# Optimization experiments

Hardware: AMD Instinct MI355X
Metric: run time of the kernel (lower is better)

Reference implementation:

```python
import jax, jax.numpy as jnp
import numpy as np

N = 100000
E = 600000
NODE_DIM = 128
EDGE_DIM = 32
HIDDEN = 128  # must equal NODE_DIM (index_add_ into zeros_like(node_features))


def _linear_params(key, fan_in, fan_out):
    kw, kb = jax.random.split(key)
    bound = 1.0 / np.sqrt(fan_in)
    W = jax.random.uniform(kw, (fan_in, fan_out), minval=-bound, maxval=bound, dtype=jnp.float32)
    b = jax.random.uniform(kb, (fan_out,), minval=-bound, maxval=bound, dtype=jnp.float32)
    return W, b


def setup_inputs() -> dict:
    key = jax.random.key(0)
    ks = jax.random.split(key, 8)
    node_features = jax.random.normal(ks[0], (N, NODE_DIM), dtype=jnp.float32)
    edge_index = jax.random.randint(ks[1], (2, E), 0, N, dtype=jnp.int32)
    edge_features = jax.random.normal(ks[2], (E, EDGE_DIM), dtype=jnp.float32)
    m_W1, m_b1 = _linear_params(ks[3], 2 * NODE_DIM + EDGE_DIM, HIDDEN)
    m_W2, m_b2 = _linear_params(ks[4], HIDDEN, HIDDEN)
    a_W, a_b = _linear_params(ks[5], HIDDEN, 1)
    u_W1, u_b1 = _linear_params(ks[6], NODE_DIM + HIDDEN, HIDDEN)
    u_W2, u_b2 = _linear_params(ks[7], HIDDEN, NODE_DIM)
    return {
        "node_features": node_features,
        "edge_features": edge_features,
        "m_W1": m_W1, "m_b1": m_b1, "m_W2": m_W2, "m_b2": m_b2,
        "a_W": a_W, "a_b": a_b,
        "u_W1": u_W1, "u_b1": u_b1, "u_W2": u_W2, "u_b2": u_b2,
        "edge_index": edge_index,
    }


def reference(node_features, edge_features, m_W1, m_b1, m_W2, m_b2,
              a_W, a_b, u_W1, u_b1, u_W2, u_b2, edge_index):
    row, col = edge_index[0], edge_index[1]
    # gather endpoints + edge feats -> [E, 2*node_dim + edge_dim]
    msg_in = jnp.concatenate([node_features[row], node_features[col], edge_features], axis=-1)
    # message MLP
    h = jax.nn.relu(msg_in @ m_W1 + m_b1)
    messages = h @ m_W2 + m_b2  # [E, hidden]
    # global softmax over all edges (dim=0), per attention column (width 1)
    attn = jax.nn.softmax(messages @ a_W + a_b, axis=0)  # [E, 1]
    messages = messages * attn
    # scatter-add into destination nodes
    aggregated = jax.ops.segment_sum(messages, col, num_segments=node_features.shape[0])
    # update MLP + residual
    upd_in = jnp.concatenate([node_features, aggregated], axis=-1)
    u = jax.nn.relu(upd_in @ u_W1 + u_b1)
    updated = u @ u_W2 + u_b2
    return updated + node_features
```

## Files before the change

kernel.cpp:

```cpp
#include <hip/hip_runtime.h>
#include <hip/hip_bf16.h>
#include <hip/hip_fp8.h>
#include <stdint.h>

#define NN 100000
#define NE 600000
#define ND 128
#define ED 32
#define HID 128
#define SCANB 391
#define NEB 4688

using short8 = __attribute__((ext_vector_type(8))) short;
using f32x4  = __attribute__((ext_vector_type(4))) float;
using f32x2  = __attribute__((ext_vector_type(2))) float;

__device__ __forceinline__ uint32_t f2bf(float f) {
  uint32_t u = __float_as_uint(f);
  return (u + 0x7FFFu + ((u >> 16) & 1u)) >> 16;
}
__device__ __forceinline__ float bf2f(uint32_t h) {
  return __uint_as_float(h << 16);
}
__device__ __forceinline__ short8 pack8(float4 a, float4 b) {
  short8 s;
  s[0] = (short)f2bf(a.x); s[1] = (short)f2bf(a.y);
  s[2] = (short)f2bf(a.z); s[3] = (short)f2bf(a.w);
  s[4] = (short)f2bf(b.x); s[5] = (short)f2bf(b.y);
  s[6] = (short)f2bf(b.z); s[7] = (short)f2bf(b.w);
  return s;
}

__device__ __forceinline__ uint8_t fp8_enc(float v) {
#if __has_builtin(__builtin_amdgcn_cvt_pk_fp8_f32)
  return (uint8_t)(__builtin_amdgcn_cvt_pk_fp8_f32(v, v, 0, false) & 0xFF);
#else
  __hip_fp8_e4m3 q(v);
  return q.__x;
#endif
}
__device__ __forceinline__ float2 fp8_dec2(uint32_t v) {
#if __has_builtin(__builtin_amdgcn_cvt_pk_f32_fp8)
  f32x2 r = __builtin_amdgcn_cvt_pk_f32_fp8((int)v, false);
  return make_float2(r[0], r[1]);
#else
  __hip_fp8_e4m3 qa, qb;
  qa.__x = (uint8_t)(v & 0xFF); qb.__x = (uint8_t)((v >> 8) & 0xFF);
  return make_float2((float)qa, (float)qb);
#endif
}
__device__ __forceinline__ long pack_fp8x8(float4 a, float4 b) {
  union { uint8_t u8[8]; long l; } u;
  u.u8[0] = fp8_enc(a.x); u.u8[1] = fp8_enc(a.y);
  u.u8[2] = fp8_enc(a.z); u.u8[3] = fp8_enc(a.w);
  u.u8[4] = fp8_enc(b.x); u.u8[5] = fp8_enc(b.y);
  u.u8[6] = fp8_enc(b.z); u.u8[7] = fp8_enc(b.w);
  return u.l;
}

__global__ __launch_bounds__(256) void k_prep_all(
    const float* __restrict__ uW1, const float* __restrict__ uW2,
    const float* __restrict__ W1, const float* __restrict__ W2,
    short* __restrict__ U1p, short* __restrict__ U2p,
    uint8_t* __restrict__ W1p8, uint8_t* __restrict__ W2p8) {
  int o = blockIdx.x * 256 + threadIdx.x;
  const float* src; int rel; int isFp8;
  short* dstS = nullptr; uint8_t* dst8 = nullptr;
  if (o < 32768)       { rel = o;         src = uW1; dstS = U1p;  isFp8 = 0; }
  else if (o < 49152)  { rel = o - 32768; src = uW2; dstS = U2p;  isFp8 = 0; }
  else if (o < 86016)  { rel = o - 49152; src = W1;  dst8 = W1p8; isFp8 = 1; }
  else if (o < 102400) { rel = o - 86016; src = W2;  dst8 = W2p8; isFp8 = 1; }
  else return;
  int j = rel & 7, c16 = (rel >> 3) & 15, g = (rel >> 7) & 3, nt = (rel >> 9) & 7, c = rel >> 12;
  int k = c * 32 + g * 8 + j, n = nt * 16 + c16;
  float v = src[k * 128 + n];
  if (isFp8) dst8[rel] = fp8_enc(v);
  else       dstS[rel] = (short)f2bf(v);
}

__global__ __launch_bounds__(256) void k_prep_nf(const float* __restrict__ nf,
                                                 short* __restrict__ nfb,
                                                 uint8_t* __restrict__ nfb8,
                                                 int* __restrict__ cnt) {
  const int total = NN * ND / 8;
  int gid = blockIdx.x * 256 + threadIdx.x;
  for (int i = gid; i < NN; i += gridDim.x * 256) cnt[i] = 0;
  for (int u = gid; u < total; u += gridDim.x * 256) {
    const float* s = nf + (size_t)u * 8;
    float4 v0 = *(const float4*)s, v1 = *(const float4*)(s + 4);
    *(short8*)(nfb + (size_t)u * 8) = pack8(v0, v1);
    uint8_t b[8];
    b[0] = fp8_enc(v0.x); b[1] = fp8_enc(v0.y); b[2] = fp8_enc(v0.z); b[3] = fp8_enc(v0.w);
    b[4] = fp8_enc(v1.x); b[5] = fp8_enc(v1.y); b[6] = fp8_enc(v1.z); b[7] = fp8_enc(v1.w);
    *(uint2*)(nfb8 + (size_t)u * 8) = *(const uint2*)b;
  }
}

__global__ __launch_bounds__(256, 4) void k_edge_mfma(
    const uint8_t* __restrict__ nfb8, const float* __restrict__ ef,
    const uint8_t* __restrict__ W1p8, const float* __restrict__ b1,
    const uint8_t* __restrict__ W2p8, const float* __restrict__ b2,
    const float* __restrict__ aW, const int* __restrict__ ei,
    const int* __restrict__ perm,
    uint8_t* __restrict__ msg8, float* __restrict__ logits) {
  __shared__ __align__(16) uint8_t sRow[128 * 136];
  __shared__ __align__(16) uint8_t sCol[128 * 136];
  __shared__ __align__(16) uint8_t sB8[4096];
  __shared__ int sIdx[256];
  __shared__ int sPerm[128];

  const int tid = threadIdx.x;
  const int wv = tid >> 6, ln = tid & 63, cr = ln & 15, gp = ln >> 4;
  const int e0 = blockIdx.x * 128;
  const int wrow = wv * 32;

  if (tid < 128) {
    int e = e0 + tid; if (e >= NE) e = NE - 1;
    sIdx[tid] = ei[e];
    sIdx[128 + tid] = ei[NE + e];
    sPerm[tid] = perm[e];
  }
  __syncthreads();

#pragma unroll
  for (int it = 0; it < 16; ++it) {
    int t = it * 256 + tid;
    int side = t >> 11;
    int r = (t & 2047) >> 4;
    int o = (t & 15) * 8;
    const uint8_t* src = nfb8 + (size_t)sIdx[side * 128 + r] * ND + o;
    uint8_t* dst = (side ? sCol : sRow) + r * 136 + o;
    *(uint2*)dst = *(const uint2*)src;
  }

  long efA0, efA1;
  {
    int ea = e0 + wrow + cr;      if (ea >= NE) ea = NE - 1;
    int eb = e0 + wrow + 16 + cr; if (eb >= NE) eb = NE - 1;
    const float* f0 = ef + (size_t)ea * ED + gp * 8;
    const float* f1 = ef + (size_t)eb * ED + gp * 8;
    efA0 = pack_fp8x8(*(const float4*)f0, *(const float4*)(f0 + 4));
    efA1 = pack_fp8x8(*(const float4*)f1, *(const float4*)(f1 + 4));
  }

  float bia[8], aWr[8], bia2[8];
#pragma unroll
  for (int nt = 0; nt < 8; ++nt) {
    bia[nt] = b1[nt * 16 + cr];
    bia2[nt] = b2[nt * 16 + cr];
    aWr[nt] = aW[nt * 16 + cr];
  }
  f32x4 acc[2][8];
#pragma unroll
  for (int mt = 0; mt < 2; ++mt)
#pragma unroll
    for (int nt = 0; nt < 8; ++nt)
      acc[mt][nt] = (f32x4){bia[nt], bia[nt], bia[nt], bia[nt]};

  for (int c = 0; c < 9; ++c) {
    __syncthreads();
    *(uint4*)&sB8[tid * 16] = *(const uint4*)(W1p8 + c * 4096 + tid * 16);
    __syncthreads();
    long af0, af1;
    if (c < 8) {
      const uint8_t* aSrc = (c < 4) ? (sRow + c * 32) : (sCol + (c - 4) * 32);
      af0 = *(const long*)(aSrc + (wrow + cr) * 136 + gp * 8);
      af1 = *(const long*)(aSrc + (wrow + 16 + cr) * 136 + gp * 8);
    } else {
      af0 = efA0; af1 = efA1;
    }
#pragma unroll
    for (int nt = 0; nt < 8; ++nt) {
      long bfr = *(const long*)&sB8[(nt * 4 + gp) * 128 + cr * 8];
      acc[0][nt] = __builtin_amdgcn_mfma_f32_16x16x32_fp8_fp8(af0, bfr, acc[0][nt], 0, 0, 0);
      acc[1][nt] = __builtin_amdgcn_mfma_f32_16x16x32_fp8_fp8(af1, bfr, acc[1][nt], 0, 0, 0);
    }
  }

#pragma unroll
  for (int mt = 0; mt < 2; ++mt)
#pragma unroll
    for (int nt = 0; nt < 8; ++nt)
#pragma unroll
      for (int rr = 0; rr < 4; ++rr)
        sRow[(wrow + mt * 16 + gp * 4 + rr) * 136 + nt * 16 + cr] =
            fp8_enc(fmaxf(acc[mt][nt][rr], 0.f));

  f32x4 acc2[2][8];
#pragma unroll
  for (int mt = 0; mt < 2; ++mt)
#pragma unroll
    for (int nt = 0; nt < 8; ++nt)
      acc2[mt][nt] = (f32x4){bia2[nt], bia2[nt], bia2[nt], bia2[nt]};
  for (int c2 = 0; c2 < 4; ++c2) {
    __syncthreads();
    *(uint4*)&sB8[tid * 16] = *(const uint4*)(W2p8 + c2 * 4096 + tid * 16);
    __syncthreads();
    long af0 = *(const long*)&sRow[(wrow + cr) * 136 + c2 * 32 + gp * 8];
    long af1 = *(const long*)&sRow[(wrow + 16 + cr) * 136 + c2 * 32 + gp * 8];
#pragma unroll
    for (int nt = 0; nt < 8; ++nt) {
      long bfr = *(const long*)&sB8[(nt * 4 + gp) * 128 + cr * 8];
      acc2[0][nt] = __builtin_amdgcn_mfma_f32_16x16x32_fp8_fp8(af0, bfr, acc2[0][nt], 0, 0, 0);
      acc2[1][nt] = __builtin_amdgcn_mfma_f32_16x16x32_fp8_fp8(af1, bfr, acc2[1][nt], 0, 0, 0);
    }
  }

#pragma unroll
  for (int mt = 0; mt < 2; ++mt)
#pragma unroll
    for (int rr = 0; rr < 4; ++rr) {
      float p = 0.f;
#pragma unroll
      for (int nt = 0; nt < 8; ++nt) p += acc2[mt][nt][rr] * aWr[nt];
      p += __shfl_xor(p, 1, 64);
      p += __shfl_xor(p, 2, 64);
      p += __shfl_xor(p, 4, 64);
      p += __shfl_xor(p, 8, 64);
      int row = wrow + mt * 16 + gp * 4 + rr;
      if (cr == 0 && e0 + row < NE) logits[sPerm[row]] = p;
    }

#pragma unroll
  for (int mt = 0; mt < 2; ++mt)
#pragma unroll
    for (int nt = 0; nt < 8; ++nt)
#pragma unroll
      for (int rr = 0; rr < 4; ++rr)
        sCol[(wrow + mt * 16 + gp * 4 + rr) * 136 + nt * 16 + cr] =
            fp8_enc(acc2[mt][nt][rr]);
  __syncthreads();
#pragma unroll
  for (int it = 0; it < 8; ++it) {
    int row = it * 16 + (tid >> 4), o8 = (tid & 15) * 8;
    if (e0 + row < NE)
      *(uint2*)(msg8 + (size_t)sPerm[row] * HID + o8) = *(const uint2*)&sCol[row * 136 + o8];
  }
}

__global__ __launch_bounds__(256, 4) void k_node_mfma(
    const short* __restrict__ nfb, const short* __restrict__ aggb,
    const short* __restrict__ U1p, const float* __restrict__ b1,
    const short* __restrict__ U2p, const float* __restrict__ b2,
    float* __restrict__ out) {
  __shared__ __align__(16) short sH[128 * 136];

  const int tid = threadIdx.x;
  const int wv = tid >> 6, ln = tid & 63, cr = ln & 15, gp = ln >> 4;
  const int n0 = blockIdx.x * 128;
  const int wrow = wv * 32;

  int na0 = n0 + wrow + cr;      if (na0 >= NN) na0 = NN - 1;
  int na1 = n0 + wrow + 16 + cr; if (na1 >= NN) na1 = NN - 1;

  float bia[8], bia2[8];
#pragma unroll
  for (int nt = 0; nt < 8; ++nt) {
    bia[nt] = b1[nt * 16 + cr];
    bia2[nt] = b2[nt * 16 + cr];
  }
  f32x4 acc[2][8];
#pragma unroll
  for (int mt = 0; mt < 2; ++mt)
#pragma unroll
    for (int nt = 0; nt < 8; ++nt)
      acc[mt][nt] = (f32x4){bia[nt], bia[nt], bia[nt], bia[nt]};

#pragma unroll
  for (int c = 0; c < 8; ++c) {
    const short* base = (c < 4) ? nfb : aggb;
    const int ko = (c & 3) * 32 + gp * 8;
    short8 af0 = *(const short8*)(base + (size_t)na0 * ND + ko);
    short8 af1 = *(const short8*)(base + (size_t)na1 * ND + ko);
    const short* Wc = U1p + c * 4096;
#pragma unroll
    for (int nt = 0; nt < 8; ++nt) {
      short8 bfr = *(const short8*)(Wc + (nt * 4 + gp) * 128 + cr * 8);
      acc[0][nt] = __builtin_amdgcn_mfma_f32_16x16x32_bf16(af0, bfr, acc[0][nt], 0, 0, 0);
      acc[1][nt] = __builtin_amdgcn_mfma_f32_16x16x32_bf16(af1, bfr, acc[1][nt], 0, 0, 0);
    }
  }

#pragma unroll
  for (int mt = 0; mt < 2; ++mt)
#pragma unroll
    for (int nt = 0; nt < 8; ++nt)
#pragma unroll
      for (int rr = 0; rr < 4; ++rr)
        sH[(wrow + mt * 16 + gp * 4 + rr) * 136 + nt * 16 + cr] =
            (short)f2bf(fmaxf(acc[mt][nt][rr], 0.f));

  f32x4 acc2[2][8];
#pragma unroll
  for (int mt = 0; mt < 2; ++mt)
#pragma unroll
    for (int nt = 0; nt < 8; ++nt)
      acc2[mt][nt] = (f32x4){bia2[nt], bia2[nt], bia2[nt], bia2[nt]};
#pragma unroll
  for (int c2 = 0; c2 < 4; ++c2) {
    short8 af0 = *(const short8*)&sH[(wrow + cr) * 136 + c2 * 32 + gp * 8];
    short8 af1 = *(const short8*)&sH[(wrow + 16 + cr) * 136 + c2 * 32 + gp * 8];
    const short* Wc = U2p + c2 * 4096;
#pragma unroll
    for (int nt = 0; nt < 8; ++nt) {
      short8 bfr = *(const short8*)(Wc + (nt * 4 + gp) * 128 + cr * 8);
      acc2[0][nt] = __builtin_amdgcn_mfma_f32_16x16x32_bf16(af0, bfr, acc2[0][nt], 0, 0, 0);
      acc2[1][nt] = __builtin_amdgcn_mfma_f32_16x16x32_bf16(af1, bfr, acc2[1][nt], 0, 0, 0);
    }
  }

#pragma unroll
  for (int mt = 0; mt < 2; ++mt)
#pragma unroll
    for (int rr = 0; rr < 4; ++rr) {
      int n = n0 + wrow + mt * 16 + gp * 4 + rr;
      if (n < NN) {
#pragma unroll
        for (int nt = 0; nt < 8; ++nt) {
          int col = nt * 16 + cr;
          float r = bf2f((uint16_t)nfb[(size_t)n * ND + col]);
          out[(size_t)n * ND + col] = acc2[mt][nt][rr] + r;
        }
      }
    }
}

__device__ __forceinline__ void ms_combine(float& m, float& s, float m2, float s2) {
  float M = fmaxf(m, m2);
  s = s * expf(m - M) + s2 * expf(m2 - M);
  m = M;
}
__device__ __forceinline__ void ms_block_reduce(float& m, float& s) {
#pragma unroll
  for (int o = 1; o < 64; o <<= 1) {
    float m2 = __shfl_xor(m, o, 64), s2 = __shfl_xor(s, o, 64);
    ms_combine(m, s, m2, s2);
  }
  __shared__ float sm[4], ss[4];
  if ((threadIdx.x & 63) == 0) { sm[threadIdx.x >> 6] = m; ss[threadIdx.x >> 6] = s; }
  __syncthreads();
  m = sm[0]; s = ss[0];
  ms_combine(m, s, sm[1], ss[1]);
  ms_combine(m, s, sm[2], ss[2]);
  ms_combine(m, s, sm[3], ss[3]);
}
__global__ __launch_bounds__(256) void k_red_p(const float* __restrict__ logits,
                                               float* __restrict__ pmax,
                                               float* __restrict__ psum) {
  float m = -3.402823466e38f, s = 0.f;
  for (int i = blockIdx.x * 256 + threadIdx.x; i < NE; i += 1024 * 256) {
    float l = logits[i];
    if (l <= m) s += expf(l - m);
    else { s = s * expf(m - l) + 1.f; m = l; }
  }
  ms_block_reduce(m, s);
  if (threadIdx.x == 0) { pmax[blockIdx.x] = m; psum[blockIdx.x] = s; }
}
__global__ __launch_bounds__(256) void k_red_f(const float* __restrict__ pmax,
                                               const float* __restrict__ psum,
                                               float* __restrict__ red) {
  float m = pmax[threadIdx.x], s = psum[threadIdx.x];
  ms_combine(m, s, pmax[threadIdx.x + 256], psum[threadIdx.x + 256]);
  ms_combine(m, s, pmax[threadIdx.x + 512], psum[threadIdx.x + 512]);
  ms_combine(m, s, pmax[threadIdx.x + 768], psum[threadIdx.x + 768]);
  ms_block_reduce(m, s);
  if (threadIdx.x == 0) { red[0] = m; red[1] = 1.0f / s; }
}

__global__ __launch_bounds__(256) void k_hist(const int* __restrict__ ei,
                                              int* __restrict__ cnt) {
  int e = blockIdx.x * 256 + threadIdx.x;
  if (e < NE) atomicAdd(&cnt[ei[NE + e]], 1);
}
__global__ __launch_bounds__(256) void k_scan_bsum(const int* __restrict__ cnt,
                                                   int* __restrict__ bsum) {
  int i = blockIdx.x * 256 + threadIdx.x;
  int v = (i < NN) ? cnt[i] : 0;
#pragma unroll
  for (int s = 1; s < 64; s <<= 1) v += __shfl_xor(v, s, 64);
  __shared__ int sv[4];
  if ((threadIdx.x & 63) == 0) sv[threadIdx.x >> 6] = v;
  __syncthreads();
  if (threadIdx.x == 0) bsum[blockIdx.x] = sv[0] + sv[1] + sv[2] + sv[3];
}
__global__ __launch_bounds__(512) void k_scan_boff(const int* __restrict__ bsum,
                                                   int* __restrict__ boff,
                                                   int* __restrict__ rowptr) {
  __shared__ int s[512];
  int t = threadIdx.x;
  int v = (t < SCANB) ? bsum[t] : 0;
  s[t] = v;
  __syncthreads();
  for (int off = 1; off < 512; off <<= 1) {
    int u = (t >= off) ? s[t - off] : 0;
    __syncthreads();
    s[t] += u;
    __syncthreads();
  }
  if (t < SCANB) boff[t] = s[t] - v;
  if (t == 0) rowptr[NN] = NE;
}
__global__ __launch_bounds__(256) void k_scan_final(int* __restrict__ cnt,
                                                    const int* __restrict__ boff,
                                                    int* __restrict__ rowptr) {
  __shared__ int s[256];
  int b = blockIdx.x, t = threadIdx.x, i = b * 256 + t;
  int v = (i < NN) ? cnt[i] : 0;
  s[t] = v;
  __syncthreads();
  for (int off = 1; off < 256; off <<= 1) {
    int u = (t >= off) ? s[t - off] : 0;
    __syncthreads();
    s[t] += u;
    __syncthreads();
  }
  int excl = s[t] - v + boff[b];
  if (i < NN) { rowptr[i] = excl; cnt[i] = excl; }
}
__global__ __launch_bounds__(256) void k_fill(const int* __restrict__ ei,
                                              int* __restrict__ cursor,
                                              int* __restrict__ perm) {
  int e = blockIdx.x * 256 + threadIdx.x;
  if (e >= NE) return;
  int c = ei[NE + e];
  int pos = atomicAdd(&cursor[c], 1);
  perm[e] = pos;
}

__global__ __launch_bounds__(256) void k_agg(
    const uint8_t* __restrict__ msg8, const float* __restrict__ logits,
    const int* __restrict__ rowptr, const float* __restrict__ red,
    short* __restrict__ aggb) {
  int n = blockIdx.x * 4 + (threadIdx.x >> 6);
  int lane = threadIdx.x & 63;
  if (n >= NN) return;
  float gm = red[0], inv = red[1];
  int i0 = rowptr[n], i1 = rowptr[n + 1];
  float a0 = 0.f, a1 = 0.f;
  for (int i = i0; i < i1; ++i) {
    float wt = expf(logits[i] - gm) * inv;
    uint32_t pk = *(const uint16_t*)(msg8 + (size_t)i * HID + lane * 2);
    float2 d = fp8_dec2(pk);
    a0 += wt * d.x;
    a1 += wt * d.y;
  }
  uint32_t packed = f2bf(a0) | (f2bf(a1) << 16);
  *(uint32_t*)(aggb + (size_t)n * ND + lane * 2) = packed;
}

extern "C" void kernel_launch(void* const* d_in, const int* in_sizes, int n_in,
                              void* d_out, int out_size, void* d_ws, size_t ws_size,
                              hipStream_t stream) {
  const float* nf  = (const float*)d_in[0];
  const float* ef  = (const float*)d_in[1];
  const float* mW1 = (const float*)d_in[2];
  const float* mb1 = (const float*)d_in[3];
  const float* mW2 = (const float*)d_in[4];
  const float* mb2 = (const float*)d_in[5];
  const float* aW  = (const float*)d_in[6];
  const float* uW1 = (const float*)d_in[8];
  const float* ub1 = (const float*)d_in[9];
  const float* uW2 = (const float*)d_in[10];
  const float* ub2 = (const float*)d_in[11];
  const int*   ei  = (const int*)d_in[12];
  float* out = (float*)d_out;

  char* ws = (char*)d_ws;
  uint8_t* msg8 = (uint8_t*)ws;
  float* logits = (float*)(ws + 76800000);
  float* pmax = (float*)(ws + 79200000);
  float* psum = pmax + 1024;
  float* red  = psum + 1024;
  uint8_t* W1p8 = (uint8_t*)(ws + 79208256);
  uint8_t* W2p8 = W1p8 + 36864;
  short* U1p = (short*)(W2p8 + 16384);
  short* U2p = U1p + 32768;
  int* rowptr = (int*)(ws + 79413056);
  int* cnt    = rowptr + (NN + 1);
  int* perm   = cnt + NN;
  int* bsum   = perm + NE;
  int* boff   = bsum + 512;
  short* nfb  = (short*)(ws + 82620000);
  uint8_t* nfb8 = (uint8_t*)(ws + 108220000);
  short* aggb = (short*)(ws + 121020000);

  k_prep_all<<<400, 256, 0, stream>>>(uW1, uW2, mW1, mW2, U1p, U2p, W1p8, W2p8);
  k_prep_nf<<<2048, 256, 0, stream>>>(nf, nfb, nfb8, cnt);
  k_hist<<<(NE + 255) / 256, 256, 0, stream>>>(ei, cnt);
  k_scan_bsum<<<SCANB, 256, 0, stream>>>(cnt, bsum);
  k_scan_boff<<<1, 512, 0, stream>>>(bsum, boff, rowptr);
  k_scan_final<<<SCANB, 256, 0, stream>>>(cnt, boff, rowptr);
  k_fill<<<(NE + 255) / 256, 256, 0, stream>>>(ei, cnt, perm);
  k_edge_mfma<<<NEB, 256, 0, stream>>>(nfb8, ef, W1p8, mb1, W2p8, mb2, aW, ei, perm,
                                       msg8, logits);
  k_red_p<<<1024, 256, 0, stream>>>(logits, pmax, psum);
  k_red_f<<<1, 256, 0, stream>>>(pmax, psum, red);
  k_agg<<<(NN + 3) / 4, 256, 0, stream>>>(msg8, logits, rowptr, red, aggb);
  k_node_mfma<<<(NN + 127) / 128, 256, 0, stream>>>(nfb, aggb, U1p, ub1, U2p, ub2, out);
}
```

Before: 294.8 us.

## Fuse aggregation into node MLP kernel and merge launch-heavy prep/reduce kernels

The CSR gather-aggregation now runs inside the node MLP kernel and writes bf16 aggregates to shared memory, so the aggb round-trip through global memory and the k_agg launch are gone. The histogram moves into k_prep_nf, and count zeroing moves into k_prep_all. The two-stage softmax reduction becomes one kernel in which the last block, found with an atomic counter, does the final combine. Together this removes several launches. The risk is lower parallelism in the aggregation: each wave now handles 32 nodes one after another, with only 782 blocks, instead of one node per wave across 25k blocks.

```diff
diff --git a/kernel.cpp b/kernel.cpp
--- a/kernel.cpp
+++ b/kernel.cpp
@@ -62,8 +62,11 @@
     const float* __restrict__ uW1, const float* __restrict__ uW2,
     const float* __restrict__ W1, const float* __restrict__ W2,
     short* __restrict__ U1p, short* __restrict__ U2p,
-    uint8_t* __restrict__ W1p8, uint8_t* __restrict__ W2p8) {
+    uint8_t* __restrict__ W1p8, uint8_t* __restrict__ W2p8,
+    int* __restrict__ cnt, int* __restrict__ counter) {
   int o = blockIdx.x * 256 + threadIdx.x;
+  if (o < NN) cnt[o] = 0;
+  if (o == 0) *counter = 0;
   const float* src; int rel; int isFp8;
   short* dstS = nullptr; uint8_t* dst8 = nullptr;
   if (o < 32768)       { rel = o;         src = uW1; dstS = U1p;  isFp8 = 0; }
@@ -81,10 +84,12 @@
 __global__ __launch_bounds__(256) void k_prep_nf(const float* __restrict__ nf,
                                                  short* __restrict__ nfb,
                                                  uint8_t* __restrict__ nfb8,
+                                                 const int* __restrict__ ei,
                                                  int* __restrict__ cnt) {
   const int total = NN * ND / 8;
   int gid = blockIdx.x * 256 + threadIdx.x;
-  for (int i = gid; i < NN; i += gridDim.x * 256) cnt[i] = 0;
+  for (int e = gid; e < NE; e += gridDim.x * 256)
+    atomicAdd(&cnt[ei[NE + e]], 1);
   for (int u = gid; u < total; u += gridDim.x * 256) {
     const float* s = nf + (size_t)u * 8;
     float4 v0 = *(const float4*)s, v1 = *(const float4*)(s + 4);
@@ -238,17 +243,36 @@
   }
 }
 
-__global__ __launch_bounds__(256, 4) void k_node_mfma(
-    const short* __restrict__ nfb, const short* __restrict__ aggb,
+__global__ __launch_bounds__(256, 4) void k_node_fused(
+    const short* __restrict__ nfb, const uint8_t* __restrict__ msg8,
+    const float* __restrict__ logits, const int* __restrict__ rowptr,
+    const float* __restrict__ red,
     const short* __restrict__ U1p, const float* __restrict__ b1,
     const short* __restrict__ U2p, const float* __restrict__ b2,
     float* __restrict__ out) {
-  __shared__ __align__(16) short sH[128 * 136];
+  __shared__ __align__(16) short sBuf[128 * 136];
 
   const int tid = threadIdx.x;
   const int wv = tid >> 6, ln = tid & 63, cr = ln & 15, gp = ln >> 4;
   const int n0 = blockIdx.x * 128;
   const int wrow = wv * 32;
+  const float gm = red[0], inv = red[1];
+
+  for (int j = 0; j < 32; ++j) {
+    int n = n0 + wrow + j;
+    if (n >= NN) break;
+    int i0 = rowptr[n], i1 = rowptr[n + 1];
+    float a0 = 0.f, a1 = 0.f;
+    for (int i = i0; i < i1; ++i) {
+      float wt = expf(logits[i] - gm) * inv;
+      uint32_t pk = *(const uint16_t*)(msg8 + (size_t)i * HID + ln * 2);
+      float2 d = fp8_dec2(pk);
+      a0 += wt * d.x;
+      a1 += wt * d.y;
+    }
+    uint32_t packed = f2bf(a0) | (f2bf(a1) << 16);
+    *(uint32_t*)&sBuf[(wrow + j) * 136 + ln * 2] = packed;
+  }
 
   int na0 = n0 + wrow + cr;      if (na0 >= NN) na0 = NN - 1;
   int na1 = n0 + wrow + 16 + cr; if (na1 >= NN) na1 = NN - 1;
@@ -268,10 +292,16 @@
 
 #pragma unroll
   for (int c = 0; c < 8; ++c) {
-    const short* base = (c < 4) ? nfb : aggb;
-    const int ko = (c & 3) * 32 + gp * 8;
-    short8 af0 = *(const short8*)(base + (size_t)na0 * ND + ko);
-    short8 af1 = *(const short8*)(base + (size_t)na1 * ND + ko);
+    short8 af0, af1;
+    if (c < 4) {
+      const int ko = c * 32 + gp * 8;
+      af0 = *(const short8*)(nfb + (size_t)na0 * ND + ko);
+      af1 = *(const short8*)(nfb + (size_t)na1 * ND + ko);
+    } else {
+      const int ko = (c - 4) * 32 + gp * 8;
+      af0 = *(const short8*)&sBuf[(wrow + cr) * 136 + ko];
+      af1 = *(const short8*)&sBuf[(wrow + 16 + cr) * 136 + ko];
+    }
     const short* Wc = U1p + c * 4096;
 #pragma unroll
     for (int nt = 0; nt < 8; ++nt) {
@@ -287,7 +317,7 @@
     for (int nt = 0; nt < 8; ++nt)
 #pragma unroll
       for (int rr = 0; rr < 4; ++rr)
-        sH[(wrow + mt * 16 + gp * 4 + rr) * 136 + nt * 16 + cr] =
+        sBuf[(wrow + mt * 16 + gp * 4 + rr) * 136 + nt * 16 + cr] =
             (short)f2bf(fmaxf(acc[mt][nt][rr], 0.f));
 
   f32x4 acc2[2][8];
@@ -298,8 +328,8 @@
       acc2[mt][nt] = (f32x4){bia2[nt], bia2[nt], bia2[nt], bia2[nt]};
 #pragma unroll
   for (int c2 = 0; c2 < 4; ++c2) {
-    short8 af0 = *(const short8*)&sH[(wrow + cr) * 136 + c2 * 32 + gp * 8];
-    short8 af1 = *(const short8*)&sH[(wrow + 16 + cr) * 136 + c2 * 32 + gp * 8];
+    short8 af0 = *(const short8*)&sBuf[(wrow + cr) * 136 + c2 * 32 + gp * 8];
+    short8 af1 = *(const short8*)&sBuf[(wrow + 16 + cr) * 136 + c2 * 32 + gp * 8];
     const short* Wc = U2p + c2 * 4096;
 #pragma unroll
     for (int nt = 0; nt < 8; ++nt) {
@@ -344,9 +374,11 @@
   ms_combine(m, s, sm[2], ss[2]);
   ms_combine(m, s, sm[3], ss[3]);
 }
-__global__ __launch_bounds__(256) void k_red_p(const float* __restrict__ logits,
-                                               float* __restrict__ pmax,
-                                               float* __restrict__ psum) {
+__global__ __launch_bounds__(256) void k_red(const float* __restrict__ logits,
+                                             float* __restrict__ pmax,
+                                             float* __restrict__ psum,
+                                             float* __restrict__ red,
+                                             int* __restrict__ counter) {
   float m = -3.402823466e38f, s = 0.f;
   for (int i = blockIdx.x * 256 + threadIdx.x; i < NE; i += 1024 * 256) {
     float l = logits[i];
@@ -354,24 +386,28 @@
     else { s = s * expf(m - l) + 1.f; m = l; }
   }
   ms_block_reduce(m, s);
-  if (threadIdx.x == 0) { pmax[blockIdx.x] = m; psum[blockIdx.x] = s; }
-}
-__global__ __launch_bounds__(256) void k_red_f(const float* __restrict__ pmax,
-                                               const float* __restrict__ psum,
-                                               float* __restrict__ red) {
-  float m = pmax[threadIdx.x], s = psum[threadIdx.x];
-  ms_combine(m, s, pmax[threadIdx.x + 256], psum[threadIdx.x + 256]);
-  ms_combine(m, s, pmax[threadIdx.x + 512], psum[threadIdx.x + 512]);
-  ms_combine(m, s, pmax[threadIdx.x + 768], psum[threadIdx.x + 768]);
-  ms_block_reduce(m, s);
-  if (threadIdx.x == 0) { red[0] = m; red[1] = 1.0f / s; }
-}
-
-__global__ __launch_bounds__(256) void k_hist(const int* __restrict__ ei,
-                                              int* __restrict__ cnt) {
-  int e = blockIdx.x * 256 + threadIdx.x;
-  if (e < NE) atomicAdd(&cnt[ei[NE + e]], 1);
-}
+  __shared__ int lastFlag;
+  if (threadIdx.x == 0) {
+    pmax[blockIdx.x] = m; psum[blockIdx.x] = s;
+    __threadfence();
+    lastFlag = (__hip_atomic_fetch_add(counter, 1, __ATOMIC_ACQ_REL,
+                                       __HIP_MEMORY_SCOPE_AGENT) == 1023);
+  }
+  __syncthreads();
+  if (!lastFlag) return;
+  int t = threadIdx.x;
+  float fm = __hip_atomic_load(&pmax[t], __ATOMIC_RELAXED, __HIP_MEMORY_SCOPE_AGENT);
+  float fs = __hip_atomic_load(&psum[t], __ATOMIC_RELAXED, __HIP_MEMORY_SCOPE_AGENT);
+#pragma unroll
+  for (int k = 1; k < 4; ++k) {
+    float m2 = __hip_atomic_load(&pmax[t + k * 256], __ATOMIC_RELAXED, __HIP_MEMORY_SCOPE_AGENT);
+    float s2 = __hip_atomic_load(&psum[t + k * 256], __ATOMIC_RELAXED, __HIP_MEMORY_SCOPE_AGENT);
+    ms_combine(fm, fs, m2, s2);
+  }
+  ms_block_reduce(fm, fs);
+  if (t == 0) { red[0] = fm; red[1] = 1.0f / fs; }
+}
+
 __global__ __launch_bounds__(256) void k_scan_bsum(const int* __restrict__ cnt,
                                                    int* __restrict__ bsum) {
   int i = blockIdx.x * 256 + threadIdx.x;
@@ -425,27 +461,6 @@
   int c = ei[NE + e];
   int pos = atomicAdd(&cursor[c], 1);
   perm[e] = pos;
-}
-
-__global__ __launch_bounds__(256) void k_agg(
-    const uint8_t* __restrict__ msg8, const float* __restrict__ logits,
-    const int* __restrict__ rowptr, const float* __restrict__ red,
-    short* __restrict__ aggb) {
-  int n = blockIdx.x * 4 + (threadIdx.x >> 6);
-  int lane = threadIdx.x & 63;
-  if (n >= NN) return;
-  float gm = red[0], inv = red[1];
-  int i0 = rowptr[n], i1 = rowptr[n + 1];
-  float a0 = 0.f, a1 = 0.f;
-  for (int i = i0; i < i1; ++i) {
-    float wt = expf(logits[i] - gm) * inv;
-    uint32_t pk = *(const uint16_t*)(msg8 + (size_t)i * HID + lane * 2);
-    float2 d = fp8_dec2(pk);
-    a0 += wt * d.x;
-    a1 += wt * d.y;
-  }
-  uint32_t packed = f2bf(a0) | (f2bf(a1) << 16);
-  *(uint32_t*)(aggb + (size_t)n * ND + lane * 2) = packed;
 }
 
 extern "C" void kernel_launch(void* const* d_in, const int* in_sizes, int n_in,
@@ -471,7 +486,8 @@
   float* pmax = (float*)(ws + 79200000);
   float* psum = pmax + 1024;
   float* red  = psum + 1024;
-  uint8_t* W1p8 = (uint8_t*)(ws + 79208256);
+  int* counter = (int*)(red + 2);
+  uint8_t* W1p8 = (uint8_t*)(ws + 79208256 + 64);
   uint8_t* W2p8 = W1p8 + 36864;
   short* U1p = (short*)(W2p8 + 16384);
   short* U2p = U1p + 32768;
@@ -482,19 +498,17 @@
   int* boff   = bsum + 512;
   short* nfb  = (short*)(ws + 82620000);
   uint8_t* nfb8 = (uint8_t*)(ws + 108220000);
-  short* aggb = (short*)(ws + 121020000);
-
-  k_prep_all<<<400, 256, 0, stream>>>(uW1, uW2, mW1, mW2, U1p, U2p, W1p8, W2p8);
-  k_prep_nf<<<2048, 256, 0, stream>>>(nf, nfb, nfb8, cnt);
-  k_hist<<<(NE + 255) / 256, 256, 0, stream>>>(ei, cnt);
+
+  k_prep_all<<<400, 256, 0, stream>>>(uW1, uW2, mW1, mW2, U1p, U2p, W1p8, W2p8,
+                                      cnt, counter);
+  k_prep_nf<<<2048, 256, 0, stream>>>(nf, nfb, nfb8, ei, cnt);
   k_scan_bsum<<<SCANB, 256, 0, stream>>>(cnt, bsum);
   k_scan_boff<<<1, 512, 0, stream>>>(bsum, boff, rowptr);
   k_scan_final<<<SCANB, 256, 0, stream>>>(cnt, boff, rowptr);
   k_fill<<<(NE + 255) / 256, 256, 0, stream>>>(ei, cnt, perm);
   k_edge_mfma<<<NEB, 256, 0, stream>>>(nfb8, ef, W1p8, mb1, W2p8, mb2, aW, ei, perm,
                                        msg8, logits);
-  k_red_p<<<1024, 256, 0, stream>>>(logits, pmax, psum);
-  k_red_f<<<1, 256, 0, stream>>>(pmax, psum, red);
-  k_agg<<<(NN + 3) / 4, 256, 0, stream>>>(msg8, logits, rowptr, red, aggb);
-  k_node_mfma<<<(NN + 127) / 128, 256, 0, stream>>>(nfb, aggb, U1p, ub1, U2p, ub2, out);
-}
+  k_red<<<1024, 256, 0, stream>>>(logits, pmax, psum, red, counter);
+  k_node_fused<<<(NN + 127) / 128, 256, 0, stream>>>(nfb, msg8, logits, rowptr,
+                                                     red, U1p, ub1, U2p, ub2, out);
+}
```

After: 348.3 us. 1.18x slower.
